# Optimization experiments

Measured on AMD Instinct MI355X. Metric: run time of the kernel, lower is better.

The kernel has to match this reference:

```python
import jax, jax.numpy as jnp
import numpy as np

N_NODES = 524288
N_EDGES = 2097152
B = 16384
CONCAT = 128 + 128 + 881  # 1137


def _glorot(key, shape):
    fan_in, fan_out = shape[0], shape[1]
    s = jnp.sqrt(6.0 / (fan_in + fan_out))
    return jax.random.uniform(key, shape, jnp.float32, -s, s)


def setup_inputs() -> dict:
    key = jax.random.key(0)
    ks = jax.random.split(key, 24)
    inp = {
        'drug_x': jax.random.normal(ks[0], (N_NODES, 30), jnp.float32),
        'edge_index': jax.random.randint(ks[1], (2, N_EDGES), 0, N_NODES, jnp.int32),
        'batch': jnp.sort(jax.random.randint(ks[2], (N_NODES,), 0, B, jnp.int32)),
        'protein_x': jax.random.normal(ks[3], (B, 979), jnp.float32),
        'fppubchem': jax.random.uniform(ks[4], (B, 881), jnp.float32),
        # GCN layers (PyG GCNConv: linear no-bias, bias added after aggregation)
        'W1': _glorot(ks[5], (30, 64)), 'b1': jnp.zeros((64,), jnp.float32),
        'W2': _glorot(ks[6], (64, 64)), 'b2': jnp.zeros((64,), jnp.float32),
        'W3': _glorot(ks[7], (64, 64)), 'b3': jnp.zeros((64,), jnp.float32),
        'fc_drug_w': _glorot(ks[8], (64, 128)), 'fc_drug_b': jnp.zeros((128,), jnp.float32),
        'fc_prot_w': _glorot(ks[9], (979, 128)), 'fc_prot_b': jnp.zeros((128,), jnp.float32),
        'fc1_w': _glorot(ks[10], (CONCAT, 512)), 'fc1_b': jnp.zeros((512,), jnp.float32),
        'fc2_w': _glorot(ks[11], (512, 256)), 'fc2_b': jnp.zeros((256,), jnp.float32),
        'fc3_w': _glorot(ks[12], (256, 1)), 'fc3_b': jnp.zeros((1,), jnp.float32),
    }
    return inp


def _gcn_layer(x, W, b, src, dst, deg_inv_sqrt, n_nodes):
    # x' = D^-1/2 (A+I) D^-1/2 (x W) + b   (src/dst already include self-loops)
    h = x @ W
    norm = deg_inv_sqrt[src] * deg_inv_sqrt[dst]  # [E+N]
    msg = h[src] * norm[:, None]
    out = jax.ops.segment_sum(msg, dst, num_segments=n_nodes)
    return out + b


def reference(drug_x, edge_index, batch, protein_x, fppubchem,
              W1, b1, W2, b2, W3, b3,
              fc_drug_w, fc_drug_b, fc_prot_w, fc_prot_b,
              fc1_w, fc1_b, fc2_w, fc2_b, fc3_w, fc3_b):
    n = drug_x.shape[0]
    loops = jnp.arange(n, dtype=edge_index.dtype)
    src = jnp.concatenate([edge_index[0], loops])
    dst = jnp.concatenate([edge_index[1], loops])
    deg = jax.ops.segment_sum(jnp.ones_like(src, jnp.float32), dst, num_segments=n)
    deg_inv_sqrt = jnp.where(deg > 0, jax.lax.rsqrt(jnp.maximum(deg, 1.0)), 0.0)

    h = jax.nn.relu(_gcn_layer(drug_x, W1, b1, src, dst, deg_inv_sqrt, n))
    h = jax.nn.relu(_gcn_layer(h, W2, b2, src, dst, deg_inv_sqrt, n))
    h = jax.nn.relu(_gcn_layer(h, W3, b3, src, dst, deg_inv_sqrt, n))

    # global mean pool over graphs
    nb = fppubchem.shape[0]
    sums = jax.ops.segment_sum(h, batch, num_segments=nb)
    cnts = jax.ops.segment_sum(jnp.ones((n,), jnp.float32), batch, num_segments=nb)
    pooled = sums / jnp.maximum(cnts, 1.0)[:, None]

    drug = jax.nn.relu(pooled @ fc_drug_w + fc_drug_b)
    prot = jax.nn.relu(protein_x @ fc_prot_w + fc_prot_b)
    comb = jnp.concatenate([drug, prot, fppubchem], axis=1)

    # fresh LayerNorm (weight=1, bias=0); dropout treated as identity (eval/deterministic)
    mu = jnp.mean(comb, axis=-1, keepdims=True)
    var = jnp.mean((comb - mu) ** 2, axis=-1, keepdims=True)
    comb = (comb - mu) * jax.lax.rsqrt(var + 1e-5)

    comb = jax.nn.relu(comb @ fc1_w + fc1_b)
    comb = jax.nn.relu(comb @ fc2_w + fc2_b)
    return comb @ fc3_w + fc3_b
```

## Files before the change

kernel.cpp:

```cpp
#include <hip/hip_runtime.h>
#include <hip/hip_bf16.h>

#define CONCAT_F 1137
#define CONCAT_P 1152
#define PROT_K 979
#define PROT_P 992

typedef __attribute__((ext_vector_type(8))) short bf16x8;
typedef __attribute__((ext_vector_type(4))) float f32x4;

static __device__ __forceinline__ float bfu2f(unsigned short u) {
  return __uint_as_float(((unsigned)u) << 16);
}
static __device__ __forceinline__ unsigned short f2bfu(float v) {
  __hip_bfloat16 t = __float2bfloat16(v);
  unsigned short u;
  __builtin_memcpy(&u, &t, 2);
  return u;
}

#define ACC4(A0, A1, A2, A3, U)        \
  {                                    \
    A0 += bfu2f((U).x & 0xffffu);      \
    A1 += bfu2f((U).x >> 16);          \
    A2 += bfu2f((U).y & 0xffffu);      \
    A3 += bfu2f((U).y >> 16);          \
  }

__global__ void k_count_xcd(const int* __restrict__ dst, int* __restrict__ rs,
                            int E, int shift, int chunk) {
  int cls = blockIdx.x & 7;
  int slice = blockIdx.x >> 3;
  int s0 = slice * chunk;
  int s1 = min(E, s0 + chunk);
  for (int e = s0 + threadIdx.x; e < s1; e += blockDim.x) {
    int d = dst[e];
    if ((d >> shift) == cls) atomicAdd(&rs[d], 1);
  }
}

__global__ void k_scatter_xcd(const int* __restrict__ src, const int* __restrict__ dst,
                              int* __restrict__ rs, int* __restrict__ csr,
                              int E, int shift, int chunk) {
  int cls = blockIdx.x & 7;
  int slice = blockIdx.x >> 3;
  int s0 = slice * chunk;
  int s1 = min(E, s0 + chunk);
  for (int e = s0 + threadIdx.x; e < s1; e += blockDim.x) {
    int d = dst[e];
    if ((d >> shift) == cls) {
      int pos = atomicAdd(&rs[d], 1);
      csr[pos] = src[e];
    }
  }
}

__global__ void k_scan_p1(const int* __restrict__ cnt, int* __restrict__ part,
                          float* __restrict__ dis, int n) {
  __shared__ int red[256];
  int tid = threadIdx.x;
  long base = (long)blockIdx.x * 1024 + tid * 4;
  int s = 0;
#pragma unroll
  for (int i = 0; i < 4; ++i) {
    long j = base + i;
    if (j < n) {
      int c = cnt[j];
      s += c;
      dis[j] = rsqrtf(1.0f + (float)c);
    }
  }
  red[tid] = s;
  __syncthreads();
  for (int off = 128; off; off >>= 1) {
    if (tid < off) red[tid] += red[tid + off];
    __syncthreads();
  }
  if (tid == 0) part[blockIdx.x] = red[0];
}

__global__ void k_scan_p2(int* __restrict__ part, int nb) {
  __shared__ int a[1024], b_[1024];
  int t = threadIdx.x;
  a[t] = (t < nb) ? part[t] : 0;
  __syncthreads();
  int* s = a;
  int* d = b_;
  for (int off = 1; off < 1024; off <<= 1) {
    d[t] = s[t] + ((t >= off) ? s[t - off] : 0);
    __syncthreads();
    int* tmp = s;
    s = d;
    d = tmp;
  }
  if (t < nb) part[t] = (t == 0) ? 0 : s[t - 1];
}

__global__ void k_scan_p3(int* __restrict__ rs, const int* __restrict__ part, int n) {
  __shared__ int a[256], b_[256];
  int tid = threadIdx.x;
  long base = (long)blockIdx.x * 1024 + tid * 4;
  int v[4];
#pragma unroll
  for (int i = 0; i < 4; ++i) {
    long j = base + i;
    v[i] = (j < n) ? rs[j] : 0;
  }
  a[tid] = v[0] + v[1] + v[2] + v[3];
  __syncthreads();
  int* s = a;
  int* d = b_;
  for (int off = 1; off < 256; off <<= 1) {
    d[tid] = s[tid] + ((tid >= off) ? s[tid - off] : 0);
    __syncthreads();
    int* t2 = s;
    s = d;
    d = t2;
  }
  int run = part[blockIdx.x] + ((tid == 0) ? 0 : s[tid - 1]);
#pragma unroll
  for (int i = 0; i < 4; ++i) {
    long j = base + i;
    if (j < n) {
      rs[j] = run;
      run += v[i];
    }
  }
}

template <int K, bool ACT>
__global__ __launch_bounds__(256) void k_mm(const void* __restrict__ Xv,
                                            const float* __restrict__ W,
                                            const float* __restrict__ bprev,
                                            const float* __restrict__ dis,
                                            unsigned short* __restrict__ M, int n) {
  __shared__ __align__(16) float hT[K][68];
  __shared__ __align__(16) float Ws[K * 64];
  __shared__ float disS[64];
  int tid = threadIdx.x;
  int rb = blockIdx.x * 64;
  for (int j = tid; j < K * 16; j += 256) ((float4*)Ws)[j] = ((const float4*)W)[j];
  if (tid < 64) disS[tid] = (rb + tid < n) ? dis[rb + tid] : 0.0f;
  __syncthreads();
  if constexpr (ACT) {
    const unsigned short* X = (const unsigned short*)Xv;
    int k = tid & 63;
    float bk = bprev[k];
#pragma unroll
    for (int r = tid >> 6; r < 64; r += 4) {
      float h = 0.0f;
      if (rb + r < n) {
        float raw = bfu2f(X[(long)(rb + r) * 64 + k]);
        h = fmaxf(fmaf(raw, disS[r], bk), 0.0f);
      }
      hT[k][r] = h;
    }
  } else {
    const float* X = (const float*)Xv;
    for (int idx = tid; idx < 64 * K; idx += 256) {
      int r = idx / K, k = idx - r * K;
      hT[k][r] = (rb + r < n) ? X[(long)(rb + r) * K + k] : 0.0f;
    }
  }
  __syncthreads();
  int rt = (tid & 15) * 4;
  int ct = (tid >> 4) * 4;
  float acc[4][4] = {};
#pragma unroll 5
  for (int k = 0; k < K; ++k) {
    float4 xr = *(const float4*)&hT[k][rt];
    float4 wr = *(const float4*)&Ws[k * 64 + ct];
    float xa[4] = {xr.x, xr.y, xr.z, xr.w};
    float wa[4] = {wr.x, wr.y, wr.z, wr.w};
#pragma unroll
    for (int i = 0; i < 4; ++i)
#pragma unroll
      for (int j = 0; j < 4; ++j) acc[i][j] = fmaf(xa[i], wa[j], acc[i][j]);
  }
#pragma unroll
  for (int i = 0; i < 4; ++i) {
    int row = rb + rt + i;
    if (row >= n) break;
    float dv = disS[rt + i];
    ushort4 pk;
    pk.x = f2bfu(acc[i][0] * dv);
    pk.y = f2bfu(acc[i][1] * dv);
    pk.z = f2bfu(acc[i][2] * dv);
    pk.w = f2bfu(acc[i][3] * dv);
    *(ushort4*)&M[(long)row * 64 + ct] = pk;
  }
}

static __device__ __forceinline__ void gather_rows(
    const int* __restrict__ rs, const int* __restrict__ csr,
    const unsigned short* __restrict__ Min, int node, int l16,
    float& A0, float& A1, float& A2, float& A3) {
  float a0, a1, a2, a3;
  float b0 = 0.f, b1 = 0.f, b2 = 0.f, b3 = 0.f;
  float c0 = 0.f, c1 = 0.f, c2 = 0.f, c3 = 0.f;
  float d0 = 0.f, d1 = 0.f, d2 = 0.f, d3 = 0.f;
  uint2 v = *(const uint2*)(Min + (size_t)node * 64 + l16 * 4);
  a0 = bfu2f(v.x & 0xffffu);
  a1 = bfu2f(v.x >> 16);
  a2 = bfu2f(v.y & 0xffffu);
  a3 = bfu2f(v.y >> 16);
  int start = (node == 0) ? 0 : rs[node - 1];
  int end = rs[node];
  int j = start;
  for (; j + 3 < end; j += 4) {
    int s0 = csr[j], s1 = csr[j + 1], s2 = csr[j + 2], s3 = csr[j + 3];
    uint2 u0 = *(const uint2*)(Min + (size_t)s0 * 64 + l16 * 4);
    uint2 u1 = *(const uint2*)(Min + (size_t)s1 * 64 + l16 * 4);
    uint2 u2 = *(const uint2*)(Min + (size_t)s2 * 64 + l16 * 4);
    uint2 u3 = *(const uint2*)(Min + (size_t)s3 * 64 + l16 * 4);
    ACC4(a0, a1, a2, a3, u0);
    ACC4(b0, b1, b2, b3, u1);
    ACC4(c0, c1, c2, c3, u2);
    ACC4(d0, d1, d2, d3, u3);
  }
  if (j + 1 < end) {
    int s0 = csr[j], s1 = csr[j + 1];
    uint2 u0 = *(const uint2*)(Min + (size_t)s0 * 64 + l16 * 4);
    uint2 u1 = *(const uint2*)(Min + (size_t)s1 * 64 + l16 * 4);
    ACC4(a0, a1, a2, a3, u0);
    ACC4(b0, b1, b2, b3, u1);
    j += 2;
  }
  if (j < end) {
    uint2 u0 = *(const uint2*)(Min + (size_t)csr[j] * 64 + l16 * 4);
    ACC4(a0, a1, a2, a3, u0);
  }
  A0 = (a0 + b0) + (c0 + d0);
  A1 = (a1 + b1) + (c1 + d1);
  A2 = (a2 + b2) + (c2 + d2);
  A3 = (a3 + b3) + (c3 + d3);
}

__global__ __launch_bounds__(256) void k_gmm(
    const int* __restrict__ rs, const int* __restrict__ csr,
    const unsigned short* __restrict__ Min, const float* __restrict__ dis,
    const float* __restrict__ bias, const float* __restrict__ W,
    unsigned short* __restrict__ Mout, int n) {
  __shared__ __align__(16) unsigned short As[64 * 64];
  __shared__ __align__(16) unsigned short Bt[64 * 64];
  const int tid = threadIdx.x;
  const int bm = blockIdx.x * 64;
  {
    int nn = tid & 63, k0 = (tid >> 6) * 16;
    bf16x8 v0, v1;
#pragma unroll
    for (int i = 0; i < 8; ++i) v0[i] = (short)f2bfu(W[(size_t)(k0 + i) * 64 + nn]);
#pragma unroll
    for (int i = 0; i < 8; ++i) v1[i] = (short)f2bfu(W[(size_t)(k0 + 8 + i) * 64 + nn]);
    int off0 = (nn * 128 + k0 * 2) ^ ((nn & 7) << 4);
    int off1 = (nn * 128 + (k0 + 8) * 2) ^ ((nn & 7) << 4);
    *(bf16x8*)((char*)Bt + off0) = v0;
    *(bf16x8*)((char*)Bt + off1) = v1;
  }
  const int lane = tid & 63;
  const int wv = tid >> 6;
  const int grp = lane >> 4, l16 = lane & 15;
  const float4 bb = *(const float4*)(bias + l16 * 4);
  for (int p = 0; p < 4; ++p) {
    int local = wv * 16 + p * 4 + grp;
    int node = bm + local;
    float A0 = 0.f, A1 = 0.f, A2 = 0.f, A3 = 0.f, dv = 0.f;
    if (node < n) {
      gather_rows(rs, csr, Min, node, l16, A0, A1, A2, A3);
      dv = dis[node];
    }
    ushort4 h;
    h.x = f2bfu(fmaxf(fmaf(A0, dv, bb.x), 0.f));
    h.y = f2bfu(fmaxf(fmaf(A1, dv, bb.y), 0.f));
    h.z = f2bfu(fmaxf(fmaf(A2, dv, bb.z), 0.f));
    h.w = f2bfu(fmaxf(fmaf(A3, dv, bb.w), 0.f));
    int off = (local * 128 + l16 * 8) ^ ((local & 7) << 4);
    *(ushort4*)((char*)As + off) = h;
  }
  __syncthreads();
  const int kb = lane >> 4, fr = lane & 15;
  f32x4 acc[4];
#pragma unroll
  for (int i = 0; i < 4; ++i) acc[i] = f32x4{0.f, 0.f, 0.f, 0.f};
  const int ar = wv * 16 + fr;
#pragma unroll
  for (int kc = 0; kc < 2; ++kc) {
    int aoff = (ar * 128 + kc * 64 + kb * 16) ^ ((ar & 7) << 4);
    bf16x8 a = *(const bf16x8*)((char*)As + aoff);
#pragma unroll
    for (int ni = 0; ni < 4; ++ni) {
      int nr = ni * 16 + fr;
      int boff = (nr * 128 + kc * 64 + kb * 16) ^ ((nr & 7) << 4);
      bf16x8 b = *(const bf16x8*)((char*)Bt + boff);
      acc[ni] = __builtin_amdgcn_mfma_f32_16x16x32_bf16(a, b, acc[ni], 0, 0, 0);
    }
  }
#pragma unroll
  for (int r = 0; r < 4; ++r) {
    int row = bm + wv * 16 + kb * 4 + r;
    if (row < n) {
      float dvo = dis[row];
#pragma unroll
      for (int ni = 0; ni < 4; ++ni)
        Mout[(size_t)row * 64 + ni * 16 + fr] = f2bfu(acc[ni][r] * dvo);
    }
  }
}

__global__ void k_gather_act(const int* __restrict__ rs, const int* __restrict__ csr,
                             const unsigned short* __restrict__ M,
                             const float* __restrict__ dis, const float* __restrict__ bias,
                             unsigned short* __restrict__ H, int n) {
  int w = (int)((blockIdx.x * (long)blockDim.x + threadIdx.x) >> 6);
  int lane = threadIdx.x & 63;
  int grp = lane >> 4, l16 = lane & 15;
  int node = w * 4 + grp;
  if (node >= n) return;
  float A0, A1, A2, A3;
  gather_rows(rs, csr, M, node, l16, A0, A1, A2, A3);
  float dv = dis[node];
  float4 bb = *(const float4*)(bias + l16 * 4);
  ushort4 o;
  o.x = f2bfu(fmaxf(fmaf(A0, dv, bb.x), 0.f));
  o.y = f2bfu(fmaxf(fmaf(A1, dv, bb.y), 0.f));
  o.z = f2bfu(fmaxf(fmaf(A2, dv, bb.z), 0.f));
  o.w = f2bfu(fmaxf(fmaf(A3, dv, bb.w), 0.f));
  *(ushort4*)(H + (size_t)node * 64 + l16 * 4) = o;
}

__global__ void k_pool8(const unsigned short* __restrict__ H, const int* __restrict__ batch,
                        float* __restrict__ sums, float* __restrict__ cntf, int n) {
  int w = (int)((blockIdx.x * (long)blockDim.x + threadIdx.x) >> 6);
  int lane = threadIdx.x & 63;
  int r0 = w * 8;
  if (r0 >= n) return;
  int cur = batch[r0];
  float acc = bfu2f(H[(long)r0 * 64 + lane]);
  float c = 1.0f;
  for (int i = 1; i < 8; ++i) {
    int r = r0 + i;
    if (r >= n) break;
    int b = batch[r];
    float v = bfu2f(H[(long)r * 64 + lane]);
    if (b == cur) {
      acc += v;
      c += 1.0f;
    } else {
      unsafeAtomicAdd(&sums[(long)cur * 64 + lane], acc);
      if (lane == 0) unsafeAtomicAdd(&cntf[cur], c);
      cur = b;
      acc = v;
      c = 1.0f;
    }
  }
  unsafeAtomicAdd(&sums[(long)cur * 64 + lane], acc);
  if (lane == 0) unsafeAtomicAdd(&cntf[cur], c);
}

__global__ void k_drugfc(const float* __restrict__ sums, const float* __restrict__ cnt,
                         const float* __restrict__ W, const float* __restrict__ b,
                         float* __restrict__ out, int B) {
  __shared__ float ps[64];
  int row = blockIdx.x;
  int tid = threadIdx.x;
  float inv = 1.0f / fmaxf(cnt[row], 1.0f);
  if (tid < 64) ps[tid] = sums[(long)row * 64 + tid] * inv;
  __syncthreads();
  float acc = b[tid];
#pragma unroll 8
  for (int k = 0; k < 64; ++k) acc = fmaf(ps[k], W[k * 128 + tid], acc);
  out[(long)row * 128 + tid] = fmaxf(acc, 0.0f);
}

__global__ void k_cvt_bf16(const float* __restrict__ X, unsigned short* __restrict__ Y,
                           int Kin, int ldout) {
  int row = blockIdx.x;
  const float* xr = X + (size_t)row * Kin;
  unsigned short* yr = Y + (size_t)row * ldout;
  for (int j = threadIdx.x; j < ldout; j += 256)
    yr[j] = (j < Kin) ? f2bfu(xr[j]) : 0;
}

template <bool SPLIT, typename OT>
__global__ __launch_bounds__(256, 3) void k_gemm2(
    const unsigned short* __restrict__ A, const float* __restrict__ W,
    const float* __restrict__ bias, OT* __restrict__ C,
    int Mrows, int N, int K, int lda, int nsteps, int chunkSteps) {
  __shared__ __align__(16) unsigned short As[2][64 * 32];
  __shared__ __align__(16) unsigned short Bs[2][128 * 32];
  const int tid = threadIdx.x;
  const int lane = tid & 63;
  const int wid = tid >> 6;
  const int bm = blockIdx.x * 64;
  const int bn = blockIdx.y * 128;
  const int kb = lane >> 4, fr = lane & 15;
  const int ss0 = blockIdx.z * chunkSteps;
  const int ss1 = min(nsteps, ss0 + chunkSteps);

  f32x4 acc[8];
#pragma unroll
  for (int j = 0; j < 8; ++j) acc[j] = f32x4{0.f, 0.f, 0.f, 0.f};

  const int ar = wid * 16 + fr;
  const int aOff = (ar * 64 + kb * 16) ^ ((ar & 7) << 4);
  int bOff[8];
#pragma unroll
  for (int ni = 0; ni < 8; ++ni) {
    int nr = ni * 16 + fr;
    bOff[ni] = (nr * 64 + kb * 16) ^ ((nr & 7) << 4);
  }
  const int arow = tid >> 2, ac = tid & 3;
  const int aW = (arow * 64 + ac * 16) ^ ((arow & 7) << 4);
  const int bn_ = tid & 127, bk0 = (tid >> 7) * 2;
  int bW[2];
#pragma unroll
  for (int p = 0; p < 2; ++p) {
    int kbb = bk0 + p;
    bW[p] = (bn_ * 64 + kbb * 16) ^ ((bn_ & 7) << 4);
  }

  bf16x8 pa;
  float pb[2][8];
  const unsigned short* aptr = A + (size_t)(bm + arow) * lda + ac * 8;

#define LOAD_STEP(S)                                              \
  {                                                               \
    int k0 = (S) * 32;                                            \
    pa = *(const bf16x8*)(aptr + k0);                             \
    _Pragma("unroll") for (int p = 0; p < 2; ++p) {               \
      _Pragma("unroll") for (int i = 0; i < 8; ++i) {             \
        int gk = k0 + (bk0 + p) * 8 + i;                          \
        pb[p][i] = (gk < K) ? W[(size_t)gk * N + bn + bn_] : 0.f; \
      }                                                           \
    }                                                             \
  }
#define STORE_STEP(BUF)                                           \
  {                                                               \
    *(bf16x8*)((char*)As[BUF] + aW) = pa;                         \
    _Pragma("unroll") for (int p = 0; p < 2; ++p) {               \
      bf16x8 v;                                                   \
      _Pragma("unroll") for (int i = 0; i < 8; ++i)               \
          v[i] = (short)f2bfu(pb[p][i]);                          \
      *(bf16x8*)((char*)Bs[BUF] + bW[p]) = v;                     \
    }                                                             \
  }

  LOAD_STEP(ss0);
  STORE_STEP(0);
  __syncthreads();
  int cur = 0;
  for (int s = ss0; s < ss1; ++s) {
    bool more = (s + 1 < ss1);
    if (more) LOAD_STEP(s + 1);
    bf16x8 a0 = *(const bf16x8*)((char*)As[cur] + aOff);
#pragma unroll
    for (int ni = 0; ni < 8; ++ni) {
      bf16x8 b = *(const bf16x8*)((char*)Bs[cur] + bOff[ni]);
      acc[ni] = __builtin_amdgcn_mfma_f32_16x16x32_bf16(a0, b, acc[ni], 0, 0, 0);
    }
    if (more) {
      STORE_STEP(cur ^ 1);
      __syncthreads();
      cur ^= 1;
    }
  }
  if constexpr (SPLIT) {
    float* Cz = (float*)C + (size_t)blockIdx.z * Mrows * N;
#pragma unroll
    for (int ni = 0; ni < 8; ++ni)
#pragma unroll
      for (int r = 0; r < 4; ++r) {
        int row = bm + wid * 16 + kb * 4 + r;
        int col = bn + ni * 16 + fr;
        Cz[(size_t)row * N + col] = acc[ni][r];
      }
  } else {
    float bv[8];
#pragma unroll
    for (int ni = 0; ni < 8; ++ni) bv[ni] = bias[bn + ni * 16 + fr];
#pragma unroll
    for (int ni = 0; ni < 8; ++ni)
#pragma unroll
      for (int r = 0; r < 4; ++r) {
        int row = bm + wid * 16 + kb * 4 + r;
        int col = bn + ni * 16 + fr;
        float x = fmaxf(acc[ni][r] + bv[ni], 0.f);
        if constexpr (__hip_internal::is_same<OT, float>::value) {
          C[(size_t)row * N + col] = x;
        } else {
          C[(size_t)row * N + col] = f2bfu(x);
        }
      }
  }
#undef LOAD_STEP
#undef STORE_STEP
}

__global__ void k_concat_ln(const float* __restrict__ drug, const float* __restrict__ protP,
                            const float* __restrict__ bp, const float* __restrict__ fpp,
                            unsigned short* __restrict__ comb, int B) {
  __shared__ float buf[CONCAT_F];
  __shared__ float rs[4], rs2[4];
  int row = blockIdx.x;
  int tid = threadIdx.x;
  const size_t MN = (size_t)B * 128;
  float s = 0.0f, s2 = 0.0f;
  for (int j = tid; j < CONCAT_F; j += 256) {
    float v;
    if (j < 128) {
      v = drug[(long)row * 128 + j];
    } else if (j < 256) {
      int c = j - 128;
      size_t o = (size_t)row * 128 + c;
      float acc = protP[o] + protP[MN + o] + protP[2 * MN + o] + protP[3 * MN + o];
      v = fmaxf(acc + bp[c], 0.0f);
    } else {
      v = fpp[(long)row * 881 + (j - 256)];
    }
    buf[j] = v;
    s += v;
    s2 += v * v;
  }
  for (int o = 32; o; o >>= 1) {
    s += __shfl_down(s, o, 64);
    s2 += __shfl_down(s2, o, 64);
  }
  int lane = tid & 63, wid = tid >> 6;
  if (lane == 0) { rs[wid] = s; rs2[wid] = s2; }
  __syncthreads();
  if (tid == 0) {
    float ts = rs[0] + rs[1] + rs[2] + rs[3];
    float ts2 = rs2[0] + rs2[1] + rs2[2] + rs2[3];
    float mu = ts / (float)CONCAT_F;
    float var = ts2 / (float)CONCAT_F - mu * mu;
    rs[0] = mu;
    rs2[0] = rsqrtf(fmaxf(var, 0.0f) + 1e-5f);
  }
  __syncthreads();
  float mu = rs[0], inv = rs2[0];
  for (int j = tid; j < CONCAT_P; j += 256) {
    unsigned short o = (j < CONCAT_F) ? f2bfu((buf[j] - mu) * inv) : 0;
    comb[(long)row * CONCAT_P + j] = o;
  }
}

__global__ void k_fc3(const float* __restrict__ X, const float* __restrict__ W,
                      const float* __restrict__ bias, float* __restrict__ out, int B) {
  int w = (int)((blockIdx.x * (long)blockDim.x + threadIdx.x) >> 6);
  int lane = threadIdx.x & 63;
  if (w >= B) return;
  float s = 0.0f;
#pragma unroll
  for (int j = 0; j < 4; ++j) s = fmaf(X[(long)w * 256 + lane + j * 64], W[lane + j * 64], s);
  for (int o = 32; o; o >>= 1) s += __shfl_down(s, o, 64);
  if (lane == 0) out[w] = s + bias[0];
}

extern "C" void kernel_launch(void* const* d_in, const int* in_sizes, int n_in,
                              void* d_out, int out_size, void* d_ws, size_t ws_size,
                              hipStream_t stream) {
  const float* drug_x = (const float*)d_in[0];
  const int* ei = (const int*)d_in[1];
  const int* batch = (const int*)d_in[2];
  const float* protein_x = (const float*)d_in[3];
  const float* fpp = (const float*)d_in[4];
  const float* W1 = (const float*)d_in[5];
  const float* b1 = (const float*)d_in[6];
  const float* W2 = (const float*)d_in[7];
  const float* b2 = (const float*)d_in[8];
  const float* W3 = (const float*)d_in[9];
  const float* b3 = (const float*)d_in[10];
  const float* Wd = (const float*)d_in[11];
  const float* bd = (const float*)d_in[12];
  const float* Wp = (const float*)d_in[13];
  const float* bp = (const float*)d_in[14];
  const float* Wf1 = (const float*)d_in[15];
  const float* bf1 = (const float*)d_in[16];
  const float* Wf2 = (const float*)d_in[17];
  const float* bf2 = (const float*)d_in[18];
  const float* Wf3 = (const float*)d_in[19];
  const float* bf3 = (const float*)d_in[20];
  float* out = (float*)d_out;

  const int N = in_sizes[0] / 30;
  const int E = in_sizes[1] / 2;
  const int B = in_sizes[4] / 881;

  int* rs = (int*)d_ws;
  float* dis = (float*)d_ws + ((size_t)N + 1);
  int* csr = (int*)d_ws + (2 * (size_t)N + 1);
  size_t oM = 2 * (size_t)N + 2 + (size_t)E;
  unsigned short* M = (unsigned short*)((float*)d_ws + oM);
  unsigned short* H = M + (size_t)N * 64;
  float* sums = (float*)d_ws + (oM + 64 * (size_t)N);
  float* cntf = sums + (size_t)B * 64;
  int* part = (int*)(cntf + B);
  unsigned short* protbh = (unsigned short*)(part + 1024);
  float* tail = (float*)d_ws;
  float* drug = tail;
  float* protP = drug + (size_t)B * 128;
  unsigned short* combh = (unsigned short*)(protP + 4 * (size_t)B * 128);
  unsigned short* act1h = combh + (size_t)B * CONCAT_P;
  float* act2 = (float*)(act1h + (size_t)B * 512);

  const int* srcIdx = ei;
  const int* dstIdx = ei + E;

  int shift = 0;
  while (((N - 1) >> shift) > 7) ++shift;
  const int CHUNK = 2048;
  int G = (E + CHUNK - 1) / CHUNK;

  k_cvt_bf16<<<B, 256, 0, stream>>>(protein_x, protbh, PROT_K, PROT_P);

  hipMemsetAsync(rs, 0, ((size_t)N + 1) * sizeof(int), stream);
  k_count_xcd<<<8 * G, 256, 0, stream>>>(dstIdx, rs, E, shift, CHUNK);
  int NB = (N + 1023) / 1024;
  k_scan_p1<<<NB, 256, 0, stream>>>(rs, part, dis, N);
  k_scan_p2<<<1, 1024, 0, stream>>>(part, NB);
  k_scan_p3<<<NB, 256, 0, stream>>>(rs, part, N);
  k_scatter_xcd<<<8 * G, 256, 0, stream>>>(srcIdx, dstIdx, rs, csr, E, shift, CHUNK);

  int mmBlocks = (N + 63) / 64;
  int gWaves = (N + 3) / 4;
  int gBlocks = (gWaves + 3) / 4;
  k_mm<30, false><<<mmBlocks, 256, 0, stream>>>(drug_x, W1, nullptr, dis, M, N);
  k_gmm<<<mmBlocks, 256, 0, stream>>>(rs, csr, M, dis, b1, W2, H, N);
  k_gmm<<<mmBlocks, 256, 0, stream>>>(rs, csr, H, dis, b2, W3, M, N);
  k_gather_act<<<gBlocks, 256, 0, stream>>>(rs, csr, M, dis, b3, H, N);

  hipMemsetAsync(sums, 0, ((size_t)B * 64 + B) * sizeof(float), stream);
  int poolWaves = (N + 7) / 8;
  k_pool8<<<(poolWaves + 3) / 4, 256, 0, stream>>>(H, batch, sums, cntf, N);

  k_drugfc<<<B, 128, 0, stream>>>(sums, cntf, Wd, bd, drug, B);
  k_gemm2<true, float><<<dim3(B / 64, 1, 4), 256, 0, stream>>>(
      protbh, Wp, nullptr, protP, B, 128, PROT_K, PROT_P, 31, 8);
  k_concat_ln<<<B, 256, 0, stream>>>(drug, protP, bp, fpp, combh, B);
  k_gemm2<false, unsigned short><<<dim3(B / 64, 4, 1), 256, 0, stream>>>(
      combh, Wf1, bf1, act1h, B, 512, CONCAT_F, CONCAT_P, 36, 36);
  k_gemm2<false, float><<<dim3(B / 64, 2, 1), 256, 0, stream>>>(
      act1h, Wf2, bf2, act2, B, 256, 512, 512, 16, 16);
  k_fc3<<<(B + 3) / 4, 256, 0, stream>>>(act2, Wf3, bf3, out, B);
}
```

Measured before the change: 792.8 us.

## Fuse final GCN gather into mean-pool kernel and widen fc1 GEMM tile

The last GCN layer's aggregation, bias and ReLU are computed inside the pooling kernel, so the third hidden activation is never written to memory or read back. Each wave handles eight consecutive nodes with one feature per lane, using a four-way unrolled neighbour gather. The GEMM kernel is templated on rows per wave, and fc1 now uses 128-row blocks so each B tile is reused across twice as many rows, with launch bounds lowered to two blocks per SM. The fused gather uses 2-byte per-lane loads instead of the earlier 16-lane vector loads, which may reduce memory efficiency, and the larger accumulator array raises register pressure.

Result: no change. 785.7 us (-0.9%).

```diff
diff --git a/kernel.cpp b/kernel.cpp
--- a/kernel.cpp
+++ b/kernel.cpp
@@ -307,53 +307,57 @@
   }
 }
 
-__global__ void k_gather_act(const int* __restrict__ rs, const int* __restrict__ csr,
-                             const unsigned short* __restrict__ M,
-                             const float* __restrict__ dis, const float* __restrict__ bias,
-                             unsigned short* __restrict__ H, int n) {
-  int w = (int)((blockIdx.x * (long)blockDim.x + threadIdx.x) >> 6);
-  int lane = threadIdx.x & 63;
-  int grp = lane >> 4, l16 = lane & 15;
-  int node = w * 4 + grp;
-  if (node >= n) return;
-  float A0, A1, A2, A3;
-  gather_rows(rs, csr, M, node, l16, A0, A1, A2, A3);
-  float dv = dis[node];
-  float4 bb = *(const float4*)(bias + l16 * 4);
-  ushort4 o;
-  o.x = f2bfu(fmaxf(fmaf(A0, dv, bb.x), 0.f));
-  o.y = f2bfu(fmaxf(fmaf(A1, dv, bb.y), 0.f));
-  o.z = f2bfu(fmaxf(fmaf(A2, dv, bb.z), 0.f));
-  o.w = f2bfu(fmaxf(fmaf(A3, dv, bb.w), 0.f));
-  *(ushort4*)(H + (size_t)node * 64 + l16 * 4) = o;
-}
-
-__global__ void k_pool8(const unsigned short* __restrict__ H, const int* __restrict__ batch,
+__global__ void k_gpool(const int* __restrict__ rs, const int* __restrict__ csr,
+                        const unsigned short* __restrict__ M, const float* __restrict__ dis,
+                        const float* __restrict__ b3, const int* __restrict__ batch,
                         float* __restrict__ sums, float* __restrict__ cntf, int n) {
   int w = (int)((blockIdx.x * (long)blockDim.x + threadIdx.x) >> 6);
   int lane = threadIdx.x & 63;
   int r0 = w * 8;
   if (r0 >= n) return;
+  float bl = b3[lane];
   int cur = batch[r0];
-  float acc = bfu2f(H[(long)r0 * 64 + lane]);
-  float c = 1.0f;
-  for (int i = 1; i < 8; ++i) {
-    int r = r0 + i;
-    if (r >= n) break;
-    int b = batch[r];
-    float v = bfu2f(H[(long)r * 64 + lane]);
+  float acc = 0.f, c = 0.f;
+  for (int i = 0; i < 8; ++i) {
+    int node = r0 + i;
+    int start = (node == 0) ? 0 : rs[node - 1];
+    int end = rs[node];
+    float a0 = bfu2f(M[(size_t)node * 64 + lane]);
+    float a1 = 0.f, a2 = 0.f, a3 = 0.f;
+    int j = start;
+    for (; j + 3 < end; j += 4) {
+      int s0 = csr[j], s1 = csr[j + 1], s2 = csr[j + 2], s3 = csr[j + 3];
+      unsigned short u0 = M[(size_t)s0 * 64 + lane];
+      unsigned short u1 = M[(size_t)s1 * 64 + lane];
+      unsigned short u2 = M[(size_t)s2 * 64 + lane];
+      unsigned short u3 = M[(size_t)s3 * 64 + lane];
+      a0 += bfu2f(u0);
+      a1 += bfu2f(u1);
+      a2 += bfu2f(u2);
+      a3 += bfu2f(u3);
+    }
+    if (j + 1 < end) {
+      unsigned short u0 = M[(size_t)csr[j] * 64 + lane];
+      unsigned short u1 = M[(size_t)csr[j + 1] * 64 + lane];
+      a0 += bfu2f(u0);
+      a1 += bfu2f(u1);
+      j += 2;
+    }
+    if (j < end) a0 += bfu2f(M[(size_t)csr[j] * 64 + lane]);
+    float h = fmaxf(fmaf((a0 + a1) + (a2 + a3), dis[node], bl), 0.f);
+    int b = batch[node];
     if (b == cur) {
-      acc += v;
-      c += 1.0f;
+      acc += h;
+      c += 1.f;
     } else {
-      unsafeAtomicAdd(&sums[(long)cur * 64 + lane], acc);
+      unsafeAtomicAdd(&sums[(size_t)cur * 64 + lane], acc);
       if (lane == 0) unsafeAtomicAdd(&cntf[cur], c);
       cur = b;
-      acc = v;
-      c = 1.0f;
-    }
-  }
-  unsafeAtomicAdd(&sums[(long)cur * 64 + lane], acc);
+      acc = h;
+      c = 1.f;
+    }
+  }
+  unsafeAtomicAdd(&sums[(size_t)cur * 64 + lane], acc);
   if (lane == 0) unsafeAtomicAdd(&cntf[cur], c);
 }
 
@@ -381,36 +385,51 @@
     yr[j] = (j < Kin) ? f2bfu(xr[j]) : 0;
 }
 
-template <bool SPLIT, typename OT>
-__global__ __launch_bounds__(256, 3) void k_gemm2(
+template <int MR, bool SPLIT, typename OT>
+__global__ __launch_bounds__(256, 2) void k_gemm2(
     const unsigned short* __restrict__ A, const float* __restrict__ W,
     const float* __restrict__ bias, OT* __restrict__ C,
     int Mrows, int N, int K, int lda, int nsteps, int chunkSteps) {
-  __shared__ __align__(16) unsigned short As[2][64 * 32];
+  constexpr int NF = MR / 16;
+  constexpr int BM = MR * 4;
+  __shared__ __align__(16) unsigned short As[2][BM * 32];
   __shared__ __align__(16) unsigned short Bs[2][128 * 32];
   const int tid = threadIdx.x;
   const int lane = tid & 63;
   const int wid = tid >> 6;
-  const int bm = blockIdx.x * 64;
+  const int bm = blockIdx.x * BM;
   const int bn = blockIdx.y * 128;
   const int kb = lane >> 4, fr = lane & 15;
   const int ss0 = blockIdx.z * chunkSteps;
   const int ss1 = min(nsteps, ss0 + chunkSteps);
 
-  f32x4 acc[8];
-#pragma unroll
-  for (int j = 0; j < 8; ++j) acc[j] = f32x4{0.f, 0.f, 0.f, 0.f};
-
-  const int ar = wid * 16 + fr;
-  const int aOff = (ar * 64 + kb * 16) ^ ((ar & 7) << 4);
+  f32x4 acc[NF][8];
+#pragma unroll
+  for (int mi = 0; mi < NF; ++mi)
+#pragma unroll
+    for (int j = 0; j < 8; ++j) acc[mi][j] = f32x4{0.f, 0.f, 0.f, 0.f};
+
+  int aOff[NF];
+#pragma unroll
+  for (int mi = 0; mi < NF; ++mi) {
+    int ar = wid * MR + mi * 16 + fr;
+    aOff[mi] = (ar * 64 + kb * 16) ^ ((ar & 7) << 4);
+  }
   int bOff[8];
 #pragma unroll
   for (int ni = 0; ni < 8; ++ni) {
     int nr = ni * 16 + fr;
     bOff[ni] = (nr * 64 + kb * 16) ^ ((nr & 7) << 4);
   }
-  const int arow = tid >> 2, ac = tid & 3;
-  const int aW = (arow * 64 + ac * 16) ^ ((arow & 7) << 4);
+  int aW[NF];
+  const unsigned short* aptrs[NF];
+#pragma unroll
+  for (int p = 0; p < NF; ++p) {
+    int ch = tid + p * 256;
+    int arow = ch >> 2, ac = ch & 3;
+    aW[p] = (arow * 64 + ac * 16) ^ ((arow & 7) << 4);
+    aptrs[p] = A + (size_t)(bm + arow) * lda + ac * 8;
+  }
   const int bn_ = tid & 127, bk0 = (tid >> 7) * 2;
   int bW[2];
 #pragma unroll
@@ -419,14 +438,14 @@
     bW[p] = (bn_ * 64 + kbb * 16) ^ ((bn_ & 7) << 4);
   }
 
-  bf16x8 pa;
+  bf16x8 pa[NF];
   float pb[2][8];
-  const unsigned short* aptr = A + (size_t)(bm + arow) * lda + ac * 8;
 
 #define LOAD_STEP(S)                                              \
   {                                                               \
     int k0 = (S) * 32;                                            \
-    pa = *(const bf16x8*)(aptr + k0);                             \
+    _Pragma("unroll") for (int p = 0; p < NF; ++p)                \
+        pa[p] = *(const bf16x8*)(aptrs[p] + k0);                  \
     _Pragma("unroll") for (int p = 0; p < 2; ++p) {               \
       _Pragma("unroll") for (int i = 0; i < 8; ++i) {             \
         int gk = k0 + (bk0 + p) * 8 + i;                          \
@@ -436,7 +455,8 @@
   }
 #define STORE_STEP(BUF)                                           \
   {                                                               \
-    *(bf16x8*)((char*)As[BUF] + aW) = pa;                         \
+    _Pragma("unroll") for (int p = 0; p < NF; ++p)                \
+        *(bf16x8*)((char*)As[BUF] + aW[p]) = pa[p];               \
     _Pragma("unroll") for (int p = 0; p < 2; ++p) {               \
       bf16x8 v;                                                   \
       _Pragma("unroll") for (int i = 0; i < 8; ++i)               \
@@ -452,11 +472,16 @@
   for (int s = ss0; s < ss1; ++s) {
     bool more = (s + 1 < ss1);
     if (more) LOAD_STEP(s + 1);
-    bf16x8 a0 = *(const bf16x8*)((char*)As[cur] + aOff);
+    bf16x8 a0[NF];
+#pragma unroll
+    for (int mi = 0; mi < NF; ++mi)
+      a0[mi] = *(const bf16x8*)((char*)As[cur] + aOff[mi]);
 #pragma unroll
     for (int ni = 0; ni < 8; ++ni) {
       bf16x8 b = *(const bf16x8*)((char*)Bs[cur] + bOff[ni]);
-      acc[ni] = __builtin_amdgcn_mfma_f32_16x16x32_bf16(a0, b, acc[ni], 0, 0, 0);
+#pragma unroll
+      for (int mi = 0; mi < NF; ++mi)
+        acc[mi][ni] = __builtin_amdgcn_mfma_f32_16x16x32_bf16(a0[mi], b, acc[mi][ni], 0, 0, 0);
     }
     if (more) {
       STORE_STEP(cur ^ 1);
@@ -467,30 +492,34 @@
   if constexpr (SPLIT) {
     float* Cz = (float*)C + (size_t)blockIdx.z * Mrows * N;
 #pragma unroll
-    for (int ni = 0; ni < 8; ++ni)
-#pragma unroll
-      for (int r = 0; r < 4; ++r) {
-        int row = bm + wid * 16 + kb * 4 + r;
-        int col = bn + ni * 16 + fr;
-        Cz[(size_t)row * N + col] = acc[ni][r];
-      }
+    for (int mi = 0; mi < NF; ++mi)
+#pragma unroll
+      for (int ni = 0; ni < 8; ++ni)
+#pragma unroll
+        for (int r = 0; r < 4; ++r) {
+          int row = bm + wid * MR + mi * 16 + kb * 4 + r;
+          int col = bn + ni * 16 + fr;
+          Cz[(size_t)row * N + col] = acc[mi][ni][r];
+        }
   } else {
     float bv[8];
 #pragma unroll
     for (int ni = 0; ni < 8; ++ni) bv[ni] = bias[bn + ni * 16 + fr];
 #pragma unroll
-    for (int ni = 0; ni < 8; ++ni)
-#pragma unroll
-      for (int r = 0; r < 4; ++r) {
-        int row = bm + wid * 16 + kb * 4 + r;
-        int col = bn + ni * 16 + fr;
-        float x = fmaxf(acc[ni][r] + bv[ni], 0.f);
-        if constexpr (__hip_internal::is_same<OT, float>::value) {
-          C[(size_t)row * N + col] = x;
-        } else {
-          C[(size_t)row * N + col] = f2bfu(x);
+    for (int mi = 0; mi < NF; ++mi)
+#pragma unroll
+      for (int ni = 0; ni < 8; ++ni)
+#pragma unroll
+        for (int r = 0; r < 4; ++r) {
+          int row = bm + wid * MR + mi * 16 + kb * 4 + r;
+          int col = bn + ni * 16 + fr;
+          float x = fmaxf(acc[mi][ni][r] + bv[ni], 0.f);
+          if constexpr (__hip_internal::is_same<OT, float>::value) {
+            C[(size_t)row * N + col] = x;
+          } else {
+            C[(size_t)row * N + col] = f2bfu(x);
+          }
         }
-      }
   }
 #undef LOAD_STEP
 #undef STORE_STEP
@@ -622,24 +651,21 @@
   k_scatter_xcd<<<8 * G, 256, 0, stream>>>(srcIdx, dstIdx, rs, csr, E, shift, CHUNK);
 
   int mmBlocks = (N + 63) / 64;
-  int gWaves = (N + 3) / 4;
-  int gBlocks = (gWaves + 3) / 4;
   k_mm<30, false><<<mmBlocks, 256, 0, stream>>>(drug_x, W1, nullptr, dis, M, N);
   k_gmm<<<mmBlocks, 256, 0, stream>>>(rs, csr, M, dis, b1, W2, H, N);
   k_gmm<<<mmBlocks, 256, 0, stream>>>(rs, csr, H, dis, b2, W3, M, N);
-  k_gather_act<<<gBlocks, 256, 0, stream>>>(rs, csr, M, dis, b3, H, N);
 
   hipMemsetAsync(sums, 0, ((size_t)B * 64 + B) * sizeof(float), stream);
   int poolWaves = (N + 7) / 8;
-  k_pool8<<<(poolWaves + 3) / 4, 256, 0, stream>>>(H, batch, sums, cntf, N);
+  k_gpool<<<(poolWaves + 3) / 4, 256, 0, stream>>>(rs, csr, M, dis, b3, batch, sums, cntf, N);
 
   k_drugfc<<<B, 128, 0, stream>>>(sums, cntf, Wd, bd, drug, B);
-  k_gemm2<true, float><<<dim3(B / 64, 1, 4), 256, 0, stream>>>(
+  k_gemm2<16, true, float><<<dim3(B / 64, 1, 4), 256, 0, stream>>>(
       protbh, Wp, nullptr, protP, B, 128, PROT_K, PROT_P, 31, 8);
   k_concat_ln<<<B, 256, 0, stream>>>(drug, protP, bp, fpp, combh, B);
-  k_gemm2<false, unsigned short><<<dim3(B / 64, 4, 1), 256, 0, stream>>>(
+  k_gemm2<32, false, unsigned short><<<dim3(B / 128, 4, 1), 256, 0, stream>>>(
       combh, Wf1, bf1, act1h, B, 512, CONCAT_F, CONCAT_P, 36, 36);
-  k_gemm2<false, float><<<dim3(B / 64, 2, 1), 256, 0, stream>>>(
+  k_gemm2<16, false, float><<<dim3(B / 64, 2, 1), 256, 0, stream>>>(
       act1h, Wf2, bf2, act2, B, 256, 512, 512, 16, 16);
   k_fc3<<<(B + 3) / 4, 256, 0, stream>>>(act2, Wf3, bf3, out, B);
 }
```
